# Kernel tuning notes

Hardware: AMD Instinct MI355X
Metric: run time of the kernel (lower is better)

## Reference

```python
import jax, jax.numpy as jnp
import numpy as np
from jax.ops import segment_sum

N_NODES = 50000
N_EDGES = 150000
IN_FEATS = 512
OUT_FEATS = 512


def setup_inputs() -> dict:
    key = jax.random.key(0)
    k1, k2, k3, k4 = jax.random.split(key, 4)
    x = jax.random.normal(k1, (N_NODES, IN_FEATS), dtype=jnp.float32)
    src = jax.random.randint(k2, (N_EDGES,), 0, N_NODES, dtype=jnp.int64)
    dst = jax.random.randint(k3, (N_EDGES,), 0, N_NODES, dtype=jnp.int64)
    # Xavier-uniform init like reset_parameters
    limit = float(np.sqrt(6.0 / (IN_FEATS + OUT_FEATS)))
    W = jax.random.uniform(k4, (IN_FEATS, OUT_FEATS), dtype=jnp.float32,
                           minval=-limit, maxval=limit)
    b = jnp.zeros((OUT_FEATS,), dtype=jnp.float32)
    return {"x": x, "src": src, "dst": dst, "W": W, "b": b}


def reference(x, src, dst, W, b):
    # DGL GraphConv with norm='both':
    #   out = relu( D_dst^{-1/2} A D_src^{-1/2} X W + b )
    # Dropout is identity in eval mode (training=False).
    ones = jnp.ones((src.shape[0],), dtype=x.dtype)
    deg_out = segment_sum(ones, src, num_segments=N_NODES)  # source out-degree
    deg_in = segment_sum(ones, dst, num_segments=N_NODES)   # dest in-degree
    norm_src = jnp.where(deg_out > 0, deg_out, 1.0) ** -0.5  # [N]
    norm_dst = jnp.where(deg_in > 0, deg_in, 1.0) ** -0.5    # [N]

    h = x * norm_src[:, None]                         # [N, in]
    agg = segment_sum(h[src], dst, num_segments=N_NODES)  # scatter-add over edges
    agg = agg * norm_dst[:, None]                     # [N, in]
    out = agg @ W + b                                 # [N, out]
    return jax.nn.relu(out)
```

## Files before the change

### kernel.cpp

```cpp
#include <hip/hip_runtime.h>
#include <hip/hip_bf16.h>

#define N_NODES 50000
#define N_PAD   50048
#define N_EDGES 150000
#define F 512
#define BM 128
#define BN 128
#define BK 32
#define NBLK 196
#define NWG  1564

typedef __attribute__((ext_vector_type(4))) float f32x4;
typedef __attribute__((ext_vector_type(4))) unsigned int u32x4;
typedef __attribute__((ext_vector_type(2))) unsigned int u32x2;

__device__ __forceinline__ unsigned short f2bf(float f) {
    unsigned int u = __float_as_uint(f);
    return (unsigned short)((u + 0x7fffu + ((u >> 16) & 1u)) >> 16);
}
__device__ __forceinline__ unsigned int pack2(float a, float b) {
    return (unsigned int)f2bf(a) | ((unsigned int)f2bf(b) << 16);
}
__device__ __forceinline__ void gload16(const void* g, void* l) {
    __builtin_amdgcn_global_load_lds(
        (const __attribute__((address_space(1))) unsigned int*)g,
        (__attribute__((address_space(3))) unsigned int*)l, 16, 0, 0);
}

__global__ void __launch_bounds__(256) crd_deg(const int* __restrict__ src,
                                               const int* __restrict__ dst,
                                               int* __restrict__ hist) {
    int e = blockIdx.x * 256 + threadIdx.x;
    if (e < N_EDGES) {
        atomicAdd(&hist[src[e]], 1);
        atomicAdd(&hist[N_NODES + dst[e]], 1);
    }
}

__global__ void __launch_bounds__(256) crd_norm(const int* __restrict__ hist,
                                                float* __restrict__ norms) {
    int i = blockIdx.x * 256 + threadIdx.x;
    if (i < 2 * N_NODES) {
        int d = hist[i];
        norms[i] = rsqrtf((float)(d > 0 ? d : 1));
    }
}

__global__ void __launch_bounds__(256) crd_bsum(const int* __restrict__ hist_in,
                                                int* __restrict__ bsum) {
    __shared__ int s[256];
    int t = threadIdx.x;
    int i = blockIdx.x * 256 + t;
    s[t] = (i < N_NODES) ? hist_in[i] : 0;
    __syncthreads();
    #pragma unroll
    for (int o = 128; o > 0; o >>= 1) {
        if (t < o) s[t] += s[t + o];
        __syncthreads();
    }
    if (t == 0) bsum[blockIdx.x] = s[0];
}

__global__ void __launch_bounds__(256) crd_bscan(const int* __restrict__ bsum,
                                                 int* __restrict__ bsumoff) {
    __shared__ int s[256];
    int t = threadIdx.x;
    int v = (t < NBLK) ? bsum[t] : 0;
    s[t] = v;
    __syncthreads();
    #pragma unroll
    for (int d = 1; d < 256; d <<= 1) {
        int add = (t >= d) ? s[t - d] : 0;
        __syncthreads();
        s[t] += add;
        __syncthreads();
    }
    if (t < NBLK) bsumoff[t] = s[t] - v;
}

__global__ void __launch_bounds__(256) crd_escan(const int* __restrict__ hist_in,
                                                 const int* __restrict__ bsumoff,
                                                 int* __restrict__ off,
                                                 int* __restrict__ cursor) {
    __shared__ int s[256];
    int t = threadIdx.x;
    int i = blockIdx.x * 256 + t;
    int v = (i < N_NODES) ? hist_in[i] : 0;
    s[t] = v;
    __syncthreads();
    #pragma unroll
    for (int d = 1; d < 256; d <<= 1) {
        int add = (t >= d) ? s[t - d] : 0;
        __syncthreads();
        s[t] += add;
        __syncthreads();
    }
    int excl = s[t] - v + bsumoff[blockIdx.x];
    if (i < N_NODES) { off[i] = excl; cursor[i] = excl; }
    if (i == N_NODES - 1) off[N_NODES] = excl + v;
}

__global__ void __launch_bounds__(256) crd_place(const int* __restrict__ src,
                                                 const int* __restrict__ dst,
                                                 int* __restrict__ cursor,
                                                 int* __restrict__ sorted) {
    int e = blockIdx.x * 256 + threadIdx.x;
    if (e < N_EDGES) {
        int slot = atomicAdd(&cursor[dst[e]], 1);
        sorted[slot] = src[e];
    }
}

__global__ void __launch_bounds__(256) crd_wt(const float* __restrict__ W,
                                              unsigned short* __restrict__ Wt) {
    int idx = blockIdx.x * 256 + threadIdx.x;
    int n = idx >> 9, k = idx & 511;
    Wt[idx] = f2bf(W[k * F + n]);
}

__global__ void __launch_bounds__(256) crd_gather(const float* __restrict__ x,
                                                  const int* __restrict__ sorted,
                                                  const int* __restrict__ off,
                                                  const float* __restrict__ norms,
                                                  unsigned short* __restrict__ aggb) {
    int gw = (blockIdx.x * 256 + threadIdx.x) >> 6;
    int lane = threadIdx.x & 63;
    int wid = gw >> 1, half = gw & 1;
    if (wid >= N_PAD) return;
    f32x4 a = {0.f,0.f,0.f,0.f}, b = a;
    if (wid < N_NODES) {
        int e0 = off[wid], e1 = off[wid + 1];
        const float* xh = x + half * 256;
        int e = e0;
        for (; e + 1 < e1; e += 2) {
            int s0 = sorted[e], s1 = sorted[e + 1];
            float ns0 = norms[s0], ns1 = norms[s1];
            a += ((const f32x4*)(xh + (size_t)s0 * F))[lane] * ns0;
            b += ((const f32x4*)(xh + (size_t)s1 * F))[lane] * ns1;
        }
        if (e < e1) {
            int s = sorted[e];
            a += ((const f32x4*)(xh + (size_t)s * F))[lane] * norms[s];
        }
        float nd = norms[N_NODES + wid];
        a = (a + b) * nd;
    }
    u32x2 w;
    w.x = pack2(a.x, a.y); w.y = pack2(a.z, a.w);
    *(u32x2*)(aggb + (size_t)wid * F + half * 256 + lane * 4) = w;
}

__global__ void __launch_bounds__(256, 3) crd_gemm(const unsigned short* __restrict__ aggb,
                                                   const unsigned short* __restrict__ Wt,
                                                   const float* __restrict__ bias,
                                                   float* __restrict__ out) {
    __shared__ __align__(16) unsigned short lA[2][4 * BM * 8];
    __shared__ __align__(16) unsigned short lB[2][4 * BN * 8];
    const int tid = threadIdx.x;
    int bid = blockIdx.x;
    int xcd = bid & 7, lid = bid >> 3;
    int swz = (xcd < 4 ? xcd * 196 : 784 + (xcd - 4) * 195) + lid;
    const int rowbase = (swz >> 2) * BM;
    const int nbase = (swz & 3) * BN;
    const int lane = tid & 63;
    const int wave = tid >> 6;
    const int wm = wave >> 1, wn = wave & 1;
    const int g = lane >> 4, r = lane & 15;

    f32x4 acc[4][4];
    #pragma unroll
    for (int i = 0; i < 4; ++i)
        #pragma unroll
        for (int j = 0; j < 4; ++j) acc[i][j] = (f32x4){0.f, 0.f, 0.f, 0.f};

#define STAGE(B, KS) do { \
    _Pragma("unroll") \
    for (int j_ = 0; j_ < 2; ++j_) { \
        int gg = j_ * 256 + tid;                  \
        int k8 = gg >> 7, rw = gg & 127; \
        gload16(aggb + (size_t)(rowbase + rw) * F + (KS) * BK + k8 * 8, \
                &lA[B][(j_ * 256 + wave * 64) * 8]); \
    } \
    _Pragma("unroll") \
    for (int j_ = 0; j_ < 2; ++j_) { \
        int gg = j_ * 256 + tid; \
        int k8 = gg >> 7, nn = gg & 127; \
        gload16(Wt + (size_t)(nbase + nn) * F + (KS) * BK + k8 * 8, \
                &lB[B][(j_ * 256 + wave * 64) * 8]); \
    } \
} while (0)

    STAGE(0, 0);
    __syncthreads();
    for (int ks = 0; ks < F / BK; ++ks) {
        int buf = ks & 1;
        if (ks + 1 < F / BK) STAGE(buf ^ 1, ks + 1);
        {
            u32x4 af[4], bfr[4];
            #pragma unroll
            for (int mi = 0; mi < 4; ++mi)
                af[mi] = *(const u32x4*)&lA[buf][(g * BM + wm * 64 + mi * 16 + r) * 8];
            #pragma unroll
            for (int ni = 0; ni < 4; ++ni)
                bfr[ni] = *(const u32x4*)&lB[buf][(g * BN + wn * 64 + ni * 16 + r) * 8];
            #pragma unroll
            for (int mi = 0; mi < 4; ++mi)
                #pragma unroll
                for (int ni = 0; ni < 4; ++ni)
                    asm("v_mfma_f32_16x16x32_bf16 %0, %1, %2, %0"
                        : "+v"(acc[mi][ni]) : "v"(bfr[ni]), "v"(af[mi]));
        }
        __syncthreads();
    }
#undef STAGE

    #pragma unroll
    for (int mi = 0; mi < 4; ++mi) {
        int row = rowbase + wm * 64 + mi * 16 + r;
        if (row < N_NODES) {
            #pragma unroll
            for (int ni = 0; ni < 4; ++ni) {
                int c0 = nbase + wn * 64 + ni * 16 + g * 4;
                f32x4 bv = *(const f32x4*)(bias + c0);
                f32x4 v = acc[mi][ni] + bv;
                v.x = fmaxf(v.x, 0.f); v.y = fmaxf(v.y, 0.f);
                v.z = fmaxf(v.z, 0.f); v.w = fmaxf(v.w, 0.f);
                *(f32x4*)(out + (size_t)row * F + c0) = v;
            }
        }
    }
}

extern "C" void kernel_launch(void* const* d_in, const int* in_sizes, int n_in,
                              void* d_out, int out_size, void* d_ws, size_t ws_size,
                              hipStream_t stream) {
    const float* x = (const float*)d_in[0];
    const int* src = (const int*)d_in[1];
    const int* dst = (const int*)d_in[2];
    const float* W = (const float*)d_in[3];
    const float* bias = (const float*)d_in[4];
    float* out = (float*)d_out;

    float* norms = (float*)d_ws;
    int* hist = (int*)(norms + 2 * N_NODES);
    int* off = hist + 2 * N_NODES;
    int* cursor = off + N_NODES + 1;
    int* sorted = cursor + N_NODES;
    int* bsum = sorted + N_EDGES;
    int* bsumoff = bsum + NBLK;
    unsigned short* Wt = (unsigned short*)
        (((uintptr_t)(bsumoff + NBLK) + 63) & ~(uintptr_t)63);
    unsigned short* aggb = Wt + (size_t)F * F;
    size_t need = (size_t)((char*)(aggb + (size_t)N_PAD * F) - (char*)d_ws);
    if (ws_size < need) {
        hipMemsetAsync(d_out, 0, (size_t)out_size * sizeof(float), stream);
        return;
    }

    hipMemsetAsync(hist, 0, 2 * N_NODES * sizeof(int), stream);
    crd_deg<<<(N_EDGES + 255) / 256, 256, 0, stream>>>(src, dst, hist);
    crd_norm<<<(2 * N_NODES + 255) / 256, 256, 0, stream>>>(hist, norms);
    crd_wt<<<(F * F) / 256, 256, 0, stream>>>(W, Wt);
    crd_bsum<<<NBLK, 256, 0, stream>>>(hist + N_NODES, bsum);
    crd_bscan<<<1, 256, 0, stream>>>(bsum, bsumoff);
    crd_escan<<<NBLK, 256, 0, stream>>>(hist + N_NODES, bsumoff, off, cursor);
    crd_place<<<(N_EDGES + 255) / 256, 256, 0, stream>>>(src, dst, cursor, sorted);
    crd_gather<<<N_PAD / 2, 256, 0, stream>>>(x, sorted, off, norms, aggb);
    crd_gemm<<<NWG, 256, 0, stream>>>(aggb, Wt, bias, out);
}
```

Baseline: 168.1 us.

## Fuse small preprocessing kernels and triple-buffer GEMM LDS pipeline

Merges the degree histogram with the W transpose/bf16 conversion into one launch, and the norm computation with the block-sum reduction into another, cutting two kernel launches. The GEMM main loop moves from double to triple buffering with explicit vmcnt waits and raw barriers, so loads run two stages ahead of compute. This raises LDS use per workgroup, which may lower occupancy, and depends on correct vmcnt accounting of the async global-to-LDS loads.

Result: faster. 163.6 us (-2.7%).

```diff
diff --git a/kernel.cpp b/kernel.cpp
--- a/kernel.cpp
+++ b/kernel.cpp
@@ -10,6 +10,8 @@
 #define BK 32
 #define NBLK 196
 #define NWG  1564
+#define DEGB 586
+#define NSTEP 16
 
 typedef __attribute__((ext_vector_type(4))) float f32x4;
 typedef __attribute__((ext_vector_type(4))) unsigned int u32x4;
@@ -28,38 +30,45 @@
         (__attribute__((address_space(3))) unsigned int*)l, 16, 0, 0);
 }
 
-__global__ void __launch_bounds__(256) crd_deg(const int* __restrict__ src,
-                                               const int* __restrict__ dst,
-                                               int* __restrict__ hist) {
-    int e = blockIdx.x * 256 + threadIdx.x;
-    if (e < N_EDGES) {
-        atomicAdd(&hist[src[e]], 1);
-        atomicAdd(&hist[N_NODES + dst[e]], 1);
-    }
-}
-
-__global__ void __launch_bounds__(256) crd_norm(const int* __restrict__ hist,
-                                                float* __restrict__ norms) {
-    int i = blockIdx.x * 256 + threadIdx.x;
+__global__ void __launch_bounds__(256) crd_deg_wt(const int* __restrict__ src,
+                                                  const int* __restrict__ dst,
+                                                  int* __restrict__ hist,
+                                                  const float* __restrict__ W,
+                                                  unsigned short* __restrict__ Wt) {
+    int b = blockIdx.x;
+    if (b < DEGB) {
+        int e = b * 256 + threadIdx.x;
+        if (e < N_EDGES) {
+            atomicAdd(&hist[src[e]], 1);
+            atomicAdd(&hist[N_NODES + dst[e]], 1);
+        }
+    } else {
+        int idx = (b - DEGB) * 256 + threadIdx.x;
+        int n = idx >> 9, k = idx & 511;
+        Wt[idx] = f2bf(W[k * F + n]);
+    }
+}
+
+__global__ void __launch_bounds__(256) crd_norm_bsum(const int* __restrict__ hist,
+                                                     float* __restrict__ norms,
+                                                     int* __restrict__ bsum) {
+    __shared__ int s[256];
+    int b = blockIdx.x, t = threadIdx.x;
+    int i = b * 256 + t;
     if (i < 2 * N_NODES) {
         int d = hist[i];
         norms[i] = rsqrtf((float)(d > 0 ? d : 1));
     }
-}
-
-__global__ void __launch_bounds__(256) crd_bsum(const int* __restrict__ hist_in,
-                                                int* __restrict__ bsum) {
-    __shared__ int s[256];
-    int t = threadIdx.x;
-    int i = blockIdx.x * 256 + t;
-    s[t] = (i < N_NODES) ? hist_in[i] : 0;
-    __syncthreads();
-    #pragma unroll
-    for (int o = 128; o > 0; o >>= 1) {
-        if (t < o) s[t] += s[t + o];
-        __syncthreads();
-    }
-    if (t == 0) bsum[blockIdx.x] = s[0];
+    if (b < NBLK) {
+        s[t] = (i < N_NODES) ? hist[N_NODES + i] : 0;
+        __syncthreads();
+        #pragma unroll
+        for (int o = 128; o > 0; o >>= 1) {
+            if (t < o) s[t] += s[t + o];
+            __syncthreads();
+        }
+        if (t == 0) bsum[b] = s[0];
+    }
 }
 
 __global__ void __launch_bounds__(256) crd_bscan(const int* __restrict__ bsum,
@@ -110,13 +119,6 @@
         int slot = atomicAdd(&cursor[dst[e]], 1);
         sorted[slot] = src[e];
     }
-}
-
-__global__ void __launch_bounds__(256) crd_wt(const float* __restrict__ W,
-                                              unsigned short* __restrict__ Wt) {
-    int idx = blockIdx.x * 256 + threadIdx.x;
-    int n = idx >> 9, k = idx & 511;
-    Wt[idx] = f2bf(W[k * F + n]);
 }
 
 __global__ void __launch_bounds__(256) crd_gather(const float* __restrict__ x,
@@ -155,8 +157,8 @@
                                                    const unsigned short* __restrict__ Wt,
                                                    const float* __restrict__ bias,
                                                    float* __restrict__ out) {
-    __shared__ __align__(16) unsigned short lA[2][4 * BM * 8];
-    __shared__ __align__(16) unsigned short lB[2][4 * BN * 8];
+    __shared__ __align__(16) unsigned short lA[3][4 * BM * 8];
+    __shared__ __align__(16) unsigned short lB[3][4 * BN * 8];
     const int tid = threadIdx.x;
     int bid = blockIdx.x;
     int xcd = bid & 7, lid = bid >> 3;
@@ -191,29 +193,36 @@
     } \
 } while (0)
 
+#define COMPUTE(B) do { \
+    u32x4 af[4], bfr[4]; \
+    _Pragma("unroll") \
+    for (int mi = 0; mi < 4; ++mi) \
+        af[mi] = *(const u32x4*)&lA[B][(g * BM + wm * 64 + mi * 16 + r) * 8]; \
+    _Pragma("unroll") \
+    for (int ni = 0; ni < 4; ++ni) \
+        bfr[ni] = *(const u32x4*)&lB[B][(g * BN + wn * 64 + ni * 16 + r) * 8]; \
+    _Pragma("unroll") \
+    for (int mi = 0; mi < 4; ++mi) \
+        _Pragma("unroll") \
+        for (int ni = 0; ni < 4; ++ni) \
+            asm("v_mfma_f32_16x16x32_bf16 %0, %1, %2, %0" \
+                : "+v"(acc[mi][ni]) : "v"(bfr[ni]), "v"(af[mi])); \
+} while (0)
+
     STAGE(0, 0);
-    __syncthreads();
-    for (int ks = 0; ks < F / BK; ++ks) {
-        int buf = ks & 1;
-        if (ks + 1 < F / BK) STAGE(buf ^ 1, ks + 1);
-        {
-            u32x4 af[4], bfr[4];
-            #pragma unroll
-            for (int mi = 0; mi < 4; ++mi)
-                af[mi] = *(const u32x4*)&lA[buf][(g * BM + wm * 64 + mi * 16 + r) * 8];
-            #pragma unroll
-            for (int ni = 0; ni < 4; ++ni)
-                bfr[ni] = *(const u32x4*)&lB[buf][(g * BN + wn * 64 + ni * 16 + r) * 8];
-            #pragma unroll
-            for (int mi = 0; mi < 4; ++mi)
-                #pragma unroll
-                for (int ni = 0; ni < 4; ++ni)
-                    asm("v_mfma_f32_16x16x32_bf16 %0, %1, %2, %0"
-                        : "+v"(acc[mi][ni]) : "v"(bfr[ni]), "v"(af[mi]));
-        }
-        __syncthreads();
+    STAGE(1, 1);
+    asm volatile("s_waitcnt vmcnt(4)" ::: "memory");
+    __builtin_amdgcn_s_barrier();
+    #pragma unroll
+    for (int t = 0; t < NSTEP; ++t) {
+        if (t + 2 < NSTEP) STAGE((t + 2) % 3, t + 2);
+        COMPUTE(t % 3);
+        if (t < NSTEP - 2) asm volatile("s_waitcnt vmcnt(4)" ::: "memory");
+        else               asm volatile("s_waitcnt vmcnt(0)" ::: "memory");
+        __builtin_amdgcn_s_barrier();
     }
 #undef STAGE
+#undef COMPUTE
 
     #pragma unroll
     for (int mi = 0; mi < 4; ++mi) {
@@ -259,10 +268,8 @@
     }
 
     hipMemsetAsync(hist, 0, 2 * N_NODES * sizeof(int), stream);
-    crd_deg<<<(N_EDGES + 255) / 256, 256, 0, stream>>>(src, dst, hist);
-    crd_norm<<<(2 * N_NODES + 255) / 256, 256, 0, stream>>>(hist, norms);
-    crd_wt<<<(F * F) / 256, 256, 0, stream>>>(W, Wt);
-    crd_bsum<<<NBLK, 256, 0, stream>>>(hist + N_NODES, bsum);
+    crd_deg_wt<<<DEGB + (F * F) / 256, 256, 0, stream>>>(src, dst, hist, W, Wt);
+    crd_norm_bsum<<<391, 256, 0, stream>>>(hist, norms, bsum);
     crd_bscan<<<1, 256, 0, stream>>>(bsum, bsumoff);
     crd_escan<<<NBLK, 256, 0, stream>>>(hist + N_NODES, bsumoff, off, cursor);
     crd_place<<<(N_EDGES + 255) / 256, 256, 0, stream>>>(src, dst, cursor, sorted);
```
